# Kernel tuning notes

Hardware: AMD Instinct MI355X
Metric: run time of the kernel (lower is better)

## Reference

```python
import jax, jax.numpy as jnp
import numpy as np

S, B, V, E, H, T = 512, 64, 100000, 128, 256, 64


def setup_inputs() -> dict:
    key = jax.random.key(0)
    ks = jax.random.split(key, 12)
    sc = 0.08  # small init scale for numerical stability
    return {
        "inputs": jax.random.randint(ks[0], (S, B), 0, V, dtype=jnp.int64),
        "emb": jax.random.normal(ks[1], (V, E), dtype=jnp.float32) * sc,
        "W_ih_f": jax.random.normal(ks[2], (4 * H, E), dtype=jnp.float32) * sc,
        "W_hh_f": jax.random.normal(ks[3], (4 * H, H), dtype=jnp.float32) * sc,
        "b_ih_f": jax.random.normal(ks[4], (4 * H,), dtype=jnp.float32) * sc,
        "b_hh_f": jax.random.normal(ks[5], (4 * H,), dtype=jnp.float32) * sc,
        "W_ih_b": jax.random.normal(ks[6], (4 * H, E), dtype=jnp.float32) * sc,
        "W_hh_b": jax.random.normal(ks[7], (4 * H, H), dtype=jnp.float32) * sc,
        "b_ih_b": jax.random.normal(ks[8], (4 * H,), dtype=jnp.float32) * sc,
        "b_hh_b": jax.random.normal(ks[9], (4 * H,), dtype=jnp.float32) * sc,
        "W_out": jax.random.normal(ks[10], (T, 2 * H), dtype=jnp.float32) * sc,
        "b_out": jax.random.normal(ks[11], (T,), dtype=jnp.float32) * sc,
    }


def _lstm_scan(x_proj, W_hh):
    # x_proj: [S, B, 4H] = input projection + biases (precomputed, hoisted out of scan)
    Bsz = x_proj.shape[1]
    Hd = W_hh.shape[1]
    h0 = jnp.zeros((Bsz, Hd), x_proj.dtype)
    c0 = jnp.zeros((Bsz, Hd), x_proj.dtype)

    def step(carry, xp):
        h, c = carry
        g = xp + h @ W_hh.T  # [B, 4H]
        i, f, gg, o = jnp.split(g, 4, axis=-1)  # PyTorch gate order: i, f, g, o
        i = jax.nn.sigmoid(i)
        f = jax.nn.sigmoid(f)
        gg = jnp.tanh(gg)
        o = jax.nn.sigmoid(o)
        c = f * c + i * gg
        h = o * jnp.tanh(c)
        return (h, c), h

    _, hs = jax.lax.scan(step, (h0, c0), x_proj)
    return hs  # [S, B, H]


def reference(inputs, emb, W_ih_f, W_hh_f, b_ih_f, b_hh_f,
              W_ih_b, W_hh_b, b_ih_b, b_hh_b, W_out, b_out):
    x = emb[inputs]  # [S, B, E] embedding gather
    # forward direction
    xf = jnp.einsum('sbe,ge->sbg', x, W_ih_f) + (b_ih_f + b_hh_f)
    hf = _lstm_scan(xf, W_hh_f)  # [S, B, H]
    # backward direction: run on time-reversed sequence, then reverse outputs
    xr = x[::-1]
    xb = jnp.einsum('sbe,ge->sbg', xr, W_ih_b) + (b_ih_b + b_hh_b)
    hb = _lstm_scan(xb, W_hh_b)[::-1]  # [S, B, H]
    hcat = jnp.concatenate([hf, hb], axis=-1)  # [S, B, 2H]
    return jnp.einsum('sbh,th->sbt', hcat, W_out) + b_out  # [S, B, T]
```

## Files before the change

### kernel.cpp

```cpp
#include <hip/hip_runtime.h>

#define S_LEN 512
#define BATCH 64
#define EDIM  128
#define HDIM  256
#define GDIM  1024
#define TDIM  64
#define NROW  32768
#define HSTR  264

typedef __attribute__((ext_vector_type(8))) short short8;
typedef __attribute__((ext_vector_type(4))) short short4v;
typedef __attribute__((ext_vector_type(4))) unsigned short us4;
typedef __attribute__((ext_vector_type(4))) float f32x4;

__device__ __forceinline__ unsigned short f2bf(float f) {
  unsigned u = __float_as_uint(f);
  u += 0x7FFFu + ((u >> 16) & 1u);
  return (unsigned short)(u >> 16);
}
__device__ __forceinline__ float bf2f(unsigned short h) {
  return __uint_as_float(((unsigned)h) << 16);
}
__device__ __forceinline__ float sigm(float x) {
  float e = __expf(-x);
  return __builtin_amdgcn_rcpf(1.f + e);
}
__device__ __forceinline__ float tanh_(float x) {
  float e = __expf(2.f * x);
  return 1.f - 2.f * __builtin_amdgcn_rcpf(e + 1.f);
}

__global__ __launch_bounds__(256) void k_pack(
    const float* __restrict__ Whf, const float* __restrict__ Whb,
    unsigned short* __restrict__ wpk, int* __restrict__ flags) {
  const int fid = blockIdx.x * 256 + threadIdx.x;
  const int l = fid & 63;
  int rest = fid >> 6;
  const int gi = rest & 3;  rest >>= 2;
  const int kk = rest & 7;  rest >>= 3;
  const int w  = rest & 3;  rest >>= 2;
  const int ch = rest & 3;  rest >>= 2;
  const int dir = rest;
  const int q = l >> 4, cl = l & 15;
  const float* Wh = dir ? Whb : Whf;
  const int row = gi * 256 + ch * 64 + w * 16 + cl;
  const float* src = Wh + (size_t)row * HDIM + kk * 32 + q * 8;
  float4 v0 = *(const float4*)src;
  float4 v1 = *(const float4*)(src + 4);
  short8 t8;
  t8[0] = (short)f2bf(v0.x); t8[1] = (short)f2bf(v0.y);
  t8[2] = (short)f2bf(v0.z); t8[3] = (short)f2bf(v0.w);
  t8[4] = (short)f2bf(v1.x); t8[5] = (short)f2bf(v1.y);
  t8[6] = (short)f2bf(v1.z); t8[7] = (short)f2bf(v1.w);
  *(short8*)(wpk + (size_t)fid * 8) = t8;
  if (blockIdx.x == 0)
    for (int i = threadIdx.x; i < 512; i += 256) flags[i] = 0;
}

__global__ __launch_bounds__(512) void k_proj(
    const int* __restrict__ tok, const float* __restrict__ emb,
    const float* __restrict__ Wf, const float* __restrict__ bihf, const float* __restrict__ bhhf,
    const float* __restrict__ Wb, const float* __restrict__ bihb, const float* __restrict__ bhhb,
    unsigned short* __restrict__ xqf, unsigned short* __restrict__ xqb) {
  __shared__ short xt[256 * 136];
  const int tid = threadIdx.x;
  const int rowbase = blockIdx.x * 256;
  const int dir = blockIdx.y;
  const float* W  = dir ? Wb   : Wf;
  const float* bi = dir ? bihb : bihf;
  const float* bh = dir ? bhhb : bhhf;
  unsigned short* xq = dir ? xqb : xqf;

  for (int i = tid; i < 256 * 32; i += 512) {
    int row = i >> 5, c4 = (i & 31) << 2;
    int t = tok[rowbase + row];
    float4 v = *(const float4*)(emb + (size_t)t * EDIM + c4);
    short4v p;
    p.x = (short)f2bf(v.x); p.y = (short)f2bf(v.y);
    p.z = (short)f2bf(v.z); p.w = (short)f2bf(v.w);
    *(short4v*)&xt[row * 136 + c4] = p;
  }
  __syncthreads();

  const int w = tid >> 6, l = tid & 63, q = l >> 4, cl = l & 15;

  short8 a[2][4];
#pragma unroll
  for (int rt = 0; rt < 2; ++rt)
#pragma unroll
    for (int kk = 0; kk < 4; ++kk)
      a[rt][kk] = *(const short8*)&xt[((2 * w + rt) * 16 + cl) * 136 + kk * 32 + q * 8];

  for (int ct = 0; ct < 64; ++ct) {
    const int colg = ct * 16 + cl;
    short8 bw[4];
#pragma unroll
    for (int kk = 0; kk < 4; ++kk) {
      const float* wp = W + (size_t)colg * EDIM + kk * 32 + q * 8;
      float4 w0 = *(const float4*)wp;
      float4 w1 = *(const float4*)(wp + 4);
      short8 t8;
      t8[0] = (short)f2bf(w0.x); t8[1] = (short)f2bf(w0.y);
      t8[2] = (short)f2bf(w0.z); t8[3] = (short)f2bf(w0.w);
      t8[4] = (short)f2bf(w1.x); t8[5] = (short)f2bf(w1.y);
      t8[6] = (short)f2bf(w1.z); t8[7] = (short)f2bf(w1.w);
      bw[kk] = t8;
    }
    float bias = bi[colg] + bh[colg];
#pragma unroll
    for (int rt = 0; rt < 2; ++rt) {
      f32x4 acc = {bias, bias, bias, bias};
#pragma unroll
      for (int kk = 0; kk < 4; ++kk)
        acc = __builtin_amdgcn_mfma_f32_16x16x32_bf16(a[rt][kk], bw[kk], acc, 0, 0, 0);
      const int rowg = rowbase + (2 * w + rt) * 16 + q * 4;
      const int s = rowg >> 6, b0 = rowg & 63;
      us4 p;
      p[0] = f2bf(acc[0]); p[1] = f2bf(acc[1]);
      p[2] = f2bf(acc[2]); p[3] = f2bf(acc[3]);
      *(us4*)&xq[((size_t)s * GDIM + colg) * BATCH + b0] = p;
    }
  }
}

__global__ __launch_bounds__(256, 1) __attribute__((amdgpu_waves_per_eu(1, 1)))
void k_lstm(
    const unsigned short* __restrict__ wpk,
    const unsigned short* __restrict__ xqf, const unsigned short* __restrict__ xqb,
    unsigned short* __restrict__ hq, unsigned short* __restrict__ hx,
    int* __restrict__ flags) {
  __shared__ short hb0[16][HSTR];
  __shared__ short hb1[16][HSTR];
  const int tid = threadIdx.x;
  const int bx = blockIdx.x;
  const int ch = bx & 3, bg = (bx >> 2) & 3, dir = bx >> 4;
  const int bxb = bx & ~3;
  const int w = tid >> 6, l = tid & 63, q = l >> 4, cl = l & 15;
  const int brow = bg * 16 + q * 4;
  const int hcol = ch * 64 + w * 16 + cl;
  const char* xqB = (const char*)(dir ? xqb : xqf);
  const char* wlp = (const char*)wpk + (size_t)((dir * 4 + ch) * 4 + w) * 32768 + l * 16;
  char* hxB = (char*)hx;

  for (int i = tid; i < 16 * HSTR; i += 256) { ((short*)hb0)[i] = 0; ((short*)hb1)[i] = 0; }

  short8 wst[8][4];
#pragma unroll
  for (int kk = 0; kk < 8; ++kk)
#pragma unroll
    for (int gi = 0; gi < 4; ++gi)
      wst[kk][gi] = *(const short8*)(wlp + (kk * 4 + gi) * 1024);

  int xlane[4];
#pragma unroll
  for (int gi = 0; gi < 4; ++gi)
    xlane[gi] = ((gi * 256 + hcol) * BATCH + brow) * 2;
  const int hq_lbyte = (brow * 512 + dir * 256 + hcol) * 2;

  const int sd  = dir ? -(GDIM * BATCH * 2) : (GDIM * BATCH * 2);
  const int hsd = dir ? -(BATCH * 512 * 2)  : (BATCH * 512 * 2);
  const int s0 = dir ? (S_LEN - 1) : 0;
  int xoff    = s0 * (GDIM * BATCH * 2);
  int hq_soff = s0 * (BATCH * 512 * 2);

  const int hx_own  = bx * 2048 + q * 512 + (w * 16 + cl) * 2;
  const int hx_prow = (tid >> 4) * 128 + (tid & 15) * 8;

  us4 xp[4];
#pragma unroll
  for (int gi = 0; gi < 4; ++gi)
    xp[gi] = *(const us4*)(xqB + xoff + xlane[gi]);
  xoff += sd;

  float cst[4] = {0.f, 0.f, 0.f, 0.f};
  __syncthreads();

#define STEP4(RB, WB, PAR, T) {                                              \
    f32x4 acc[4];                                                            \
    const f32x4 zz = {0.f, 0.f, 0.f, 0.f};                                   \
    acc[0] = zz; acc[1] = zz; acc[2] = zz; acc[3] = zz;                      \
    _Pragma("unroll") for (int kk = 0; kk < 8; ++kk) {                       \
      short8 av = *(const short8*)&RB[cl][kk * 32 + q * 8];                  \
      _Pragma("unroll") for (int gi = 0; gi < 4; ++gi)                       \
        acc[gi] = __builtin_amdgcn_mfma_f32_16x16x32_bf16(av, wst[kk][gi], acc[gi], 0, 0, 0); \
    }                                                                        \
    _Pragma("unroll") for (int r = 0; r < 4; ++r) {                          \
      float gi_ = sigm(acc[0][r] + bf2f(xp[0][r]));                          \
      float gf  = sigm(acc[1][r] + bf2f(xp[1][r]));                          \
      float gg  = tanh_(acc[2][r] + bf2f(xp[2][r]));                         \
      float go  = sigm(acc[3][r] + bf2f(xp[3][r]));                          \
      float cn = gf * cst[r] + gi_ * gg;                                     \
      cst[r] = cn;                                                           \
      unsigned short hbv = f2bf(go * tanh_(cn));                             \
      WB[q * 4 + r][hcol] = (short)hbv;                                      \
      *(unsigned short*)(hxB + (PAR) * 65536 + hx_own + r * 128) = hbv;      \
      *(unsigned short*)((char*)hq + hq_soff + hq_lbyte + r * 1024) = hbv;   \
    }                                                                        \
    hq_soff += hsd;                                                          \
    asm volatile("s_waitcnt vmcnt(0)" ::: "memory");                         \
    __builtin_amdgcn_s_barrier();                                            \
    if (tid == 0)                                                            \
      __hip_atomic_store(&flags[bx * 16], (T) + 1, __ATOMIC_RELEASE,         \
                         __HIP_MEMORY_SCOPE_AGENT);                          \
    if (tid < 3) {                                                           \
      const int pc = (tid < ch) ? tid : tid + 1;                             \
      while (__hip_atomic_load(&flags[(bxb + pc) * 16], __ATOMIC_ACQUIRE,    \
                               __HIP_MEMORY_SCOPE_AGENT) < (T) + 1) {}       \
    }                                                                        \
    __builtin_amdgcn_s_barrier();                                            \
    _Pragma("unroll") for (int p = 0; p < 3; ++p) {                          \
      const int pc = (p < ch) ? p : p + 1;                                   \
      us4 ph = *(const us4*)(hxB + (PAR) * 65536 + (bxb + pc) * 2048 + hx_prow); \
      *(us4*)&WB[tid >> 4][pc * 64 + (tid & 15) * 4] = ph;                   \
    }                                                                        \
    _Pragma("unroll") for (int gi = 0; gi < 4; ++gi)                         \
      xp[gi] = *(const us4*)(xqB + xoff + xlane[gi]);                        \
    if ((T) < S_LEN - 2) xoff += sd;                                         \
    asm volatile("s_waitcnt lgkmcnt(0)\n\ts_barrier" ::: "memory");          \
  }

  for (int it = 0; it < S_LEN / 2; ++it) {
    const int t = 2 * it;
    STEP4(hb0, hb1, 0, t);
    STEP4(hb1, hb0, 1, t + 1);
  }
#undef STEP4
}

__global__ __launch_bounds__(256) void k_out(
    const unsigned short* __restrict__ hq, const float* __restrict__ Wo,
    const float* __restrict__ bo, float* __restrict__ out) {
  __shared__ short wlds[64 * 520];
  const int tid = threadIdx.x;
  for (int i = tid; i < 64 * 128; i += 256) {
    int row = i >> 7, c4 = (i & 127) << 2;
    float4 v = *(const float4*)(Wo + (size_t)row * 512 + c4);
    short4v p;
    p.x = (short)f2bf(v.x); p.y = (short)f2bf(v.y);
    p.z = (short)f2bf(v.z); p.w = (short)f2bf(v.w);
    *(short4v*)&wlds[row * 520 + c4] = p;
  }
  __syncthreads();

  const int w = tid >> 6, l = tid & 63, q = l >> 4, cl = l & 15;
  const int rtb = blockIdx.x * 64 + w * 16;

  short8 a[16];
#pragma unroll
  for (int kk = 0; kk < 16; ++kk)
    a[kk] = *(const short8*)&hq[(size_t)(rtb + cl) * 512 + kk * 32 + q * 8];

#pragma unroll
  for (int ct = 0; ct < 4; ++ct) {
    float bias = bo[ct * 16 + cl];
    f32x4 acc = {bias, bias, bias, bias};
#pragma unroll
    for (int kk = 0; kk < 16; ++kk) {
      short8 b = *(const short8*)&wlds[(ct * 16 + cl) * 520 + kk * 32 + q * 8];
      acc = __builtin_amdgcn_mfma_f32_16x16x32_bf16(a[kk], b, acc, 0, 0, 0);
    }
#pragma unroll
    for (int r = 0; r < 4; ++r)
      out[(size_t)(rtb + q * 4 + r) * TDIM + ct * 16 + cl] = acc[r];
  }
}

extern "C" void kernel_launch(void* const* d_in, const int* in_sizes, int n_in,
                              void* d_out, int out_size, void* d_ws, size_t ws_size,
                              hipStream_t stream) {
  const int*   tok  = (const int*)d_in[0];
  const float* emb  = (const float*)d_in[1];
  const float* Wihf = (const float*)d_in[2];
  const float* Whhf = (const float*)d_in[3];
  const float* bihf = (const float*)d_in[4];
  const float* bhhf = (const float*)d_in[5];
  const float* Wihb = (const float*)d_in[6];
  const float* Whhb = (const float*)d_in[7];
  const float* bihb = (const float*)d_in[8];
  const float* bhhb = (const float*)d_in[9];
  const float* Wo   = (const float*)d_in[10];
  const float* bo   = (const float*)d_in[11];
  float* out = (float*)d_out;

  char* ws = (char*)d_ws;
  unsigned short* xqf = (unsigned short*)ws;
  unsigned short* xqb = (unsigned short*)(ws + (size_t)NROW * GDIM * 2);
  unsigned short* hq  = (unsigned short*)(ws + (size_t)NROW * GDIM * 4);
  unsigned short* wpk   = (unsigned short*)d_out;
  unsigned short* hx    = (unsigned short*)((char*)d_out + (2u << 20));
  int*            flags = (int*)((char*)d_out + (4u << 20));

  k_pack<<<256, 256, 0, stream>>>(Whhf, Whhb, wpk, flags);
  k_proj<<<dim3(128, 2), 512, 0, stream>>>(tok, emb, Wihf, bihf, bhhf,
                                           Wihb, bihb, bhhb, xqf, xqb);
  k_lstm<<<32, 256, 0, stream>>>(wpk, xqf, xqb, hq, hx, flags);
  k_out<<<512, 256, 0, stream>>>(hq, Wo, bo, out);
}
```

Before: 1.777 ms.

## Pack h exchange into 64-bit atomics and relax cross-block flag synchronization

Remaps block indices so each direction and batch group occupies adjacent block IDs. Each lane now packs its four bf16 hidden values into one 64-bit relaxed atomic store to the exchange buffer instead of four scalar stores. The hq output stores are moved after the flag publish so they leave the critical path. Every thread now spins on the three peer flags itself with relaxed loads, which removes the second barrier, and peer values are read back as 64-bit atomics. This cuts per-step synchronization latency in the recurrent loop, but dropping the release/acquire ordering relies on the hardware ordering the stores and loads correctly, which risks visibility races.

```diff
diff --git a/kernel.cpp b/kernel.cpp
--- a/kernel.cpp
+++ b/kernel.cpp
@@ -13,6 +13,7 @@
 typedef __attribute__((ext_vector_type(4))) short short4v;
 typedef __attribute__((ext_vector_type(4))) unsigned short us4;
 typedef __attribute__((ext_vector_type(4))) float f32x4;
+typedef unsigned long long ull;
 
 __device__ __forceinline__ unsigned short f2bf(float f) {
   unsigned u = __float_as_uint(f);
@@ -134,8 +135,8 @@
   __shared__ short hb1[16][HSTR];
   const int tid = threadIdx.x;
   const int bx = blockIdx.x;
-  const int ch = bx & 3, bg = (bx >> 2) & 3, dir = bx >> 4;
-  const int bxb = bx & ~3;
+  const int dir = bx & 1, ch = (bx >> 1) & 3, bg = bx >> 3;
+  const int bxb8 = bx & ~7;
   const int w = tid >> 6, l = tid & 63, q = l >> 4, cl = l & 15;
   const int brow = bg * 16 + q * 4;
   const int hcol = ch * 64 + w * 16 + cl;
@@ -164,8 +165,8 @@
   int xoff    = s0 * (GDIM * BATCH * 2);
   int hq_soff = s0 * (BATCH * 512 * 2);
 
-  const int hx_own  = bx * 2048 + q * 512 + (w * 16 + cl) * 2;
-  const int hx_prow = (tid >> 4) * 128 + (tid & 15) * 8;
+  const int hx_own = bx * 2048 + (w * 16 + cl) * 32 + q * 8;
+  const int gc = tid >> 2, grg = tid & 3;
 
   us4 xp[4];
 #pragma unroll
@@ -185,6 +186,7 @@
       _Pragma("unroll") for (int gi = 0; gi < 4; ++gi)                       \
         acc[gi] = __builtin_amdgcn_mfma_f32_16x16x32_bf16(av, wst[kk][gi], acc[gi], 0, 0, 0); \
     }                                                                        \
+    ull hpack = 0;                                                           \
     _Pragma("unroll") for (int r = 0; r < 4; ++r) {                          \
       float gi_ = sigm(acc[0][r] + bf2f(xp[0][r]));                          \
       float gf  = sigm(acc[1][r] + bf2f(xp[1][r]));                          \
@@ -194,25 +196,37 @@
       cst[r] = cn;                                                           \
       unsigned short hbv = f2bf(go * tanh_(cn));                             \
       WB[q * 4 + r][hcol] = (short)hbv;                                      \
-      *(unsigned short*)(hxB + (PAR) * 65536 + hx_own + r * 128) = hbv;      \
-      *(unsigned short*)((char*)hq + hq_soff + hq_lbyte + r * 1024) = hbv;   \
+      hpack |= (ull)hbv << (16 * r);                                         \
     }                                                                        \
-    hq_soff += hsd;                                                          \
+    __hip_atomic_store((ull*)(hxB + (PAR) * 65536 + hx_own), hpack,          \
+                       __ATOMIC_RELAXED, __HIP_MEMORY_SCOPE_AGENT);          \
     asm volatile("s_waitcnt vmcnt(0)" ::: "memory");                         \
     __builtin_amdgcn_s_barrier();                                            \
+    asm volatile("" ::: "memory");                                           \
     if (tid == 0)                                                            \
-      __hip_atomic_store(&flags[bx * 16], (T) + 1, __ATOMIC_RELEASE,         \
+      __hip_atomic_store(&flags[bx * 16], (T) + 1, __ATOMIC_RELAXED,         \
                          __HIP_MEMORY_SCOPE_AGENT);                          \
-    if (tid < 3) {                                                           \
-      const int pc = (tid < ch) ? tid : tid + 1;                             \
-      while (__hip_atomic_load(&flags[(bxb + pc) * 16], __ATOMIC_ACQUIRE,    \
+    asm volatile("" ::: "memory");                                           \
+         \
+    _Pragma("unroll") for (int r = 0; r < 4; ++r)                            \
+      *(unsigned short*)((char*)hq + hq_soff + hq_lbyte + r * 1024) =        \
+          (unsigned short)(hpack >> (16 * r));                               \
+    hq_soff += hsd;                                                          \
+    _Pragma("unroll") for (int p = 0; p < 3; ++p) {                          \
+      const int pc = (p < ch) ? p : p + 1;                                   \
+      const int pbx = bxb8 + pc * 2 + dir;                                   \
+      while (__hip_atomic_load(&flags[pbx * 16], __ATOMIC_RELAXED,           \
                                __HIP_MEMORY_SCOPE_AGENT) < (T) + 1) {}       \
     }                                                                        \
-    __builtin_amdgcn_s_barrier();                                            \
+    asm volatile("" ::: "memory");                                           \
     _Pragma("unroll") for (int p = 0; p < 3; ++p) {                          \
       const int pc = (p < ch) ? p : p + 1;                                   \
-      us4 ph = *(const us4*)(hxB + (PAR) * 65536 + (bxb + pc) * 2048 + hx_prow); \
-      *(us4*)&WB[tid >> 4][pc * 64 + (tid & 15) * 4] = ph;                   \
+      const int pbx = bxb8 + pc * 2 + dir;                                   \
+      ull v = __hip_atomic_load(                                             \
+          (const ull*)(hxB + (PAR) * 65536 + pbx * 2048 + gc * 32 + grg * 8),\
+          __ATOMIC_RELAXED, __HIP_MEMORY_SCOPE_AGENT);                       \
+      _Pragma("unroll") for (int j = 0; j < 4; ++j)                          \
+        WB[grg * 4 + j][pc * 64 + gc] = (short)(unsigned short)(v >> (16 * j)); \
     }                                                                        \
     _Pragma("unroll") for (int gi = 0; gi < 4; ++gi)                         \
       xp[gi] = *(const us4*)(xqB + xoff + xlane[gi]);                        \
```

Result: slower. 1.965 ms (+10.6%).
